# Kernel optimization log

Hardware: AMD Instinct MI355X
Metric: run time of the kernel (lower is better)

## Reference

```python
import jax, jax.numpy as jnp
import numpy as np

H = 1024      # hidden_size
NH = 16       # num_heads
HD = H // NH  # head_dim = 64
BUCKETS = 256
MAXREL = 512
SPAN = BUCKETS  # pos_ebd_size (position_buckets > 0)
B, S = 2, 2048


def setup_inputs() -> dict:
    key = jax.random.key(0)
    ks = jax.random.split(key, 10)
    s = 0.02
    return {
        'hidden_states': jax.random.normal(ks[0], (B, S, H), jnp.float32),
        'Wq': jax.random.normal(ks[1], (H, H), jnp.float32) * s, 'bq': jnp.zeros((H,), jnp.float32),
        'Wk': jax.random.normal(ks[2], (H, H), jnp.float32) * s, 'bk': jnp.zeros((H,), jnp.float32),
        'Wv': jax.random.normal(ks[3], (H, H), jnp.float32) * s, 'bv': jnp.zeros((H,), jnp.float32),
        'Wo': jax.random.normal(ks[4], (H, H), jnp.float32) * s, 'bo': jnp.zeros((H,), jnp.float32),
        'Wpk': jax.random.normal(ks[5], (H, H), jnp.float32) * s, 'bpk': jnp.zeros((H,), jnp.float32),
        'Wpq': jax.random.normal(ks[6], (H, H), jnp.float32) * s, 'bpq': jnp.zeros((H,), jnp.float32),
        'rel_emb': jax.random.normal(ks[7], (2 * SPAN, H), jnp.float32) * s,
        'ln_g': jnp.ones((H,), jnp.float32), 'ln_b': jnp.zeros((H,), jnp.float32),
    }


def _log_bucket(rel, bucket_size, max_position):
    # Faithful port of make_log_bucket_position
    sign = jnp.sign(rel).astype(jnp.float32)
    mid = bucket_size // 2
    abs_pos = jnp.where((rel < mid) & (rel > -mid), mid - 1, jnp.abs(rel)).astype(jnp.float32)
    log_pos = jnp.ceil(jnp.log(abs_pos / mid) / np.float32(np.log((max_position - 1) / mid)) * (mid - 1)) + mid
    bucket = jnp.where(abs_pos <= mid, rel.astype(jnp.float32), log_pos * sign)
    return bucket.astype(jnp.int32)


def _split_heads(x, b, s):
    # [B,S,H] -> [B,NH,S,HD]
    return x.reshape(b, s, NH, HD).transpose(0, 2, 1, 3)


def reference(hidden_states, Wq, bq, Wk, bk, Wv, bv, Wo, bo, Wpk, bpk, Wpq, bpq, rel_emb, ln_g, ln_b):
    b, s, _ = hidden_states.shape
    q = _split_heads(hidden_states @ Wq + bq, b, s)
    k = _split_heads(hidden_states @ Wk + bk, b, s)
    v = _split_heads(hidden_states @ Wv + bv, b, s)
    # scale_factor = 1 + ('c2p') + ('p2c') = 3
    scale = jnp.sqrt(jnp.asarray(HD * 3, jnp.float32))
    scores = jnp.einsum('bhqd,bhkd->bhqk', q, k) / scale
    # log-bucketed relative positions [S, S]
    ids = jnp.arange(s)
    rel = _log_bucket(ids[:, None] - ids[None, :], BUCKETS, MAXREL)
    # LayerNorm over rel embeddings (biased variance, eps=1e-5)
    mu = rel_emb.mean(-1, keepdims=True)
    var = rel_emb.var(-1, keepdims=True)
    re = (rel_emb - mu) / jnp.sqrt(var + 1e-5) * ln_g + ln_b   # [2*SPAN, H]
    pos_k = (re @ Wpk + bpk).reshape(2 * SPAN, NH, HD).transpose(1, 0, 2)  # [NH, 2*SPAN, HD]
    pos_q = (re @ Wpq + bpq).reshape(2 * SPAN, NH, HD).transpose(1, 0, 2)
    # c2p: content->position
    c2p = jnp.einsum('bhqd,hpd->bhqp', q, pos_k)                 # [B,NH,S,2*SPAN]
    c2p_idx = jnp.clip(rel + SPAN, 0, 2 * SPAN - 1)              # [S,S]
    c2p = jnp.take_along_axis(c2p, jnp.broadcast_to(c2p_idx[None, None], (b, NH, s, s)), axis=-1) / scale
    # p2c: position->content (gather on key axis, then transpose)
    p2c = jnp.einsum('bhkd,hpd->bhkp', k, pos_q)                 # [B,NH,S,2*SPAN]
    p2c_idx = jnp.clip(-rel + SPAN, 0, 2 * SPAN - 1)
    p2c = jnp.take_along_axis(p2c, jnp.broadcast_to(p2c_idx[None, None], (b, NH, s, s)), axis=-1)
    p2c = jnp.swapaxes(p2c, -1, -2) / scale
    scores = scores + c2p + p2c
    probs = jax.nn.softmax(scores.astype(jnp.float32), axis=-1).astype(q.dtype)
    ctx = jnp.einsum('bhqk,bhkd->bhqd', probs, v)
    ctx = ctx.transpose(0, 2, 1, 3).reshape(b, s, H)
    return ctx @ Wo + bo
```

## Files before the change

kernel.cpp:

```cpp
#include <hip/hip_runtime.h>

typedef unsigned short u16;
typedef unsigned int u32;
typedef unsigned long long u64;
typedef __attribute__((ext_vector_type(8))) short short8;
typedef __attribute__((ext_vector_type(4))) float float4v;

#define MFMA16(a, b, c) __builtin_amdgcn_mfma_f32_16x16x32_bf16((a), (b), (c), 0, 0, 0)

__device__ __forceinline__ u16 f2b(float x) {
    union { float f; unsigned u; } v; v.f = x;
    unsigned r = v.u + 0x7FFFu + ((v.u >> 16) & 1u);
    return (u16)(r >> 16);
}
__device__ __forceinline__ float b2f(u16 u) {
    union { unsigned u; float f; } v; v.u = ((unsigned)u) << 16; return v.f;
}

#define NH 16
#define S  2048
#define HD 64
#define H  1024
#define SC 0.10412111829775301f

#define OFF_REB   0ull
#define OFF_HSB   (OFF_REB  + 1048576ull)
#define OFF_WT    (OFF_HSB  + 8388608ull)
#define OFF_QB    (OFF_WT   + 12582912ull)
#define OFF_KB    (OFF_QB   + 8388608ull)
#define OFF_VT    (OFF_KB   + 8388608ull)
#define OFF_PKB   (OFF_VT   + 8388608ull)
#define OFF_PQB   (OFF_PKB  + 1048576ull)
#define OFF_C2P   (OFF_PQB  + 1048576ull)
#define OFF_P2CK  (OFF_C2P  + 67108864ull)
#define OFF_CTX   (OFF_P2CK + 67108864ull)
#define OFF_IDX   (OFF_CTX  + 8388608ull)
#define OFF_PF    (OFF_IDX  + 8192ull)
#define OFF_SP    (OFF_PF   + 262144ull)
#define SP_OHALF  4194304ull
#define SP_LBASE  (OFF_SP + 67108864ull)
#define SP_LHALF  65536ull
#define WS_NEED_SPLIT (SP_LBASE + 524288ull)

__global__ void k_build_idx(short* __restrict__ t) {
    int i = blockIdx.x * 256 + threadIdx.x;
    if (i >= 1024) return;
    int rel = i - 512;
    float fr = (float)rel;
    float abs_pos = (rel < 128 && rel > -128) ? 127.0f : fabsf(fr);
    const float LOGC = 1.3843393262841284f;
    float log_pos = ceilf(logf(abs_pos * (1.0f / 128.0f)) / LOGC * 127.0f) + 128.0f;
    float sgn = (fr > 0.f) ? 1.f : ((fr < 0.f) ? -1.f : 0.f);
    float bf = (abs_pos <= 128.0f) ? fr : log_pos * sgn;
    int idx = (int)bf + 256;
    idx = idx < 0 ? 0 : (idx > 511 ? 511 : idx);
    t[i] = (short)idx;
}

__global__ __launch_bounds__(256) void k_ln(const float* __restrict__ re,
                                            const float* __restrict__ g,
                                            const float* __restrict__ be,
                                            u16* __restrict__ out) {
    int row = blockIdx.x;
    const float4* x4 = (const float4*)(re + (size_t)row * H);
    int tid = threadIdx.x;
    float4 vv = x4[tid];
    float s = vv.x + vv.y + vv.z + vv.w;
    float s2 = vv.x * vv.x + vv.y * vv.y + vv.z * vv.z + vv.w * vv.w;
    for (int m = 1; m < 64; m <<= 1) {
        s += __shfl_xor(s, m, 64);
        s2 += __shfl_xor(s2, m, 64);
    }
    __shared__ float as[4], as2[4];
    if ((tid & 63) == 0) { as[tid >> 6] = s; as2[tid >> 6] = s2; }
    __syncthreads();
    s = as[0] + as[1] + as[2] + as[3];
    s2 = as2[0] + as2[1] + as2[2] + as2[3];
    float mu = s * (1.f / 1024.f);
    float var = s2 * (1.f / 1024.f) - mu * mu;
    float rstd = rsqrtf(var + 1e-5f);
    float4 gg = ((const float4*)g)[tid];
    float4 bb = ((const float4*)be)[tid];
    ushort4 r4;
    r4.x = f2b((vv.x - mu) * rstd * gg.x + bb.x);
    r4.y = f2b((vv.y - mu) * rstd * gg.y + bb.y);
    r4.z = f2b((vv.z - mu) * rstd * gg.z + bb.z);
    r4.w = f2b((vv.w - mu) * rstd * gg.w + bb.w);
    ((ushort4*)(out + (size_t)row * H))[tid] = r4;
}

__global__ __launch_bounds__(256) void k_cast(const float* __restrict__ x, u16* __restrict__ y) {
    int i = blockIdx.x * 256 + threadIdx.x;
    float4 v = ((const float4*)x)[i];
    ushort4 r;
    r.x = f2b(v.x); r.y = f2b(v.y); r.z = f2b(v.z); r.w = f2b(v.w);
    ((ushort4*)y)[i] = r;
}

__global__ __launch_bounds__(256) void k_wt6(const float* __restrict__ W0, const float* __restrict__ W1,
                                             const float* __restrict__ W2, const float* __restrict__ W3,
                                             const float* __restrict__ W4, const float* __restrict__ W5,
                                             u16* __restrict__ T0, u16* __restrict__ T1,
                                             u16* __restrict__ T2, u16* __restrict__ T3,
                                             u16* __restrict__ T4, u16* __restrict__ T5) {
    const float* W; u16* WT;
    switch (blockIdx.z) {
        case 0: W = W0; WT = T0; break;
        case 1: W = W1; WT = T1; break;
        case 2: W = W2; WT = T2; break;
        case 3: W = W3; WT = T3; break;
        case 4: W = W4; WT = T4; break;
        default: W = W5; WT = T5; break;
    }
    __shared__ float t[64][65];
    int k0 = blockIdx.x * 64, n0 = blockIdx.y * 64;
    int tid = threadIdx.x;
#pragma unroll
    for (int i = 0; i < 16; i++) {
        int lin = tid + 256 * i;
        int r = lin >> 6, c = lin & 63;
        t[r][c] = W[(size_t)(k0 + r) * H + n0 + c];
    }
    __syncthreads();
#pragma unroll
    for (int i = 0; i < 16; i++) {
        int lin = tid + 256 * i;
        int r = lin >> 6, c = lin & 63;
        WT[(size_t)(n0 + r) * H + k0 + c] = f2b(t[c][r]);
    }
}

template <int MODE>
__device__ __forceinline__ void gemm2_body(const u16* __restrict__ A,
                                           const u16* __restrict__ Bt,
                                           const float* __restrict__ bias,
                                           void* __restrict__ C, int N, int K) {
    __shared__ __align__(16) u16 As[128 * 32];
    __shared__ __align__(16) u16 Bs[128 * 32];
    int tid = threadIdx.x;
    int lane = tid & 63, w = tid >> 6;
    int ln = lane & 15, quad = lane >> 4;
    int m0 = blockIdx.x * 128, n0 = blockIdx.y * 128;
    int wm = (w >> 1) * 64, wn = (w & 1) * 64;
    float4v acc[4][4];
    float4v zero = {0.f, 0.f, 0.f, 0.f};
#pragma unroll
    for (int mi = 0; mi < 4; mi++)
#pragma unroll
        for (int ni = 0; ni < 4; ni++) acc[mi][ni] = zero;

    int r1 = tid >> 2, o1 = (tid & 3) * 8;
    const u16* ga1 = A + (size_t)(m0 + r1) * K + o1;
    const u16* gb1 = Bt + (size_t)(n0 + r1) * K + o1;
    u16* sa1 = &As[r1 * 32 + o1];
    u16* sb1 = &Bs[r1 * 32 + o1];
    size_t step2 = (size_t)64 * K;

    for (int k0 = 0; k0 < K; k0 += 32) {
        short8 va1 = *(const short8*)(ga1 + k0);
        short8 va2 = *(const short8*)(ga1 + step2 + k0);
        short8 vb1 = *(const short8*)(gb1 + k0);
        short8 vb2 = *(const short8*)(gb1 + step2 + k0);
        __syncthreads();
        *(short8*)sa1 = va1; *(short8*)(sa1 + 2048) = va2;
        *(short8*)sb1 = vb1; *(short8*)(sb1 + 2048) = vb2;
        __syncthreads();
        short8 af[4], bf[4];
#pragma unroll
        for (int mi = 0; mi < 4; mi++)
            af[mi] = *(const short8*)&As[(wm + mi * 16 + ln) * 32 + quad * 8];
#pragma unroll
        for (int ni = 0; ni < 4; ni++)
            bf[ni] = *(const short8*)&Bs[(wn + ni * 16 + ln) * 32 + quad * 8];
#pragma unroll
        for (int mi = 0; mi < 4; mi++)
#pragma unroll
            for (int ni = 0; ni < 4; ni++)
                acc[mi][ni] = MFMA16(af[mi], bf[ni], acc[mi][ni]);
    }

#pragma unroll
    for (int mi = 0; mi < 4; mi++) {
        int row0 = m0 + wm + mi * 16 + quad * 4;
#pragma unroll
        for (int ni = 0; ni < 4; ni++) {
            int col = n0 + wn + ni * 16 + ln;
            float bv = bias[col];
            if (MODE == 0) {
                u16* Cb = (u16*)C;
#pragma unroll
                for (int r = 0; r < 4; r++)
                    Cb[(size_t)(row0 + r) * N + col] = f2b(acc[mi][ni][r] + bv);
            } else if (MODE == 1) {
                float* Cf = (float*)C;
#pragma unroll
                for (int r = 0; r < 4; r++)
                    Cf[(size_t)(row0 + r) * N + col] = acc[mi][ni][r] + bv;
            } else if (MODE == 2) {
                u16* Cb = (u16*)C;
                int bb = row0 >> 11, s = row0 & 2047;
                ushort4 r4;
                r4.x = f2b(acc[mi][ni][0] + bv);
                r4.y = f2b(acc[mi][ni][1] + bv);
                r4.z = f2b(acc[mi][ni][2] + bv);
                r4.w = f2b(acc[mi][ni][3] + bv);
                *(ushort4*)(Cb + ((size_t)(bb * 1024 + col)) * 2048 + s) = r4;
            } else {
                u16* Cb = (u16*)C;
                int bb = row0 >> 11, s = row0 & 2047;
                int h = col >> 6, d = col & 63;
#pragma unroll
                for (int r = 0; r < 4; r++)
                    Cb[((size_t)(bb * 16 + h) * 2048 + s + r) * 64 + d] = f2b(acc[mi][ni][r] + bv);
            }
        }
    }
}

template <int MODE>
__global__ __launch_bounds__(256) void k_gemm2(const u16* __restrict__ A, const u16* __restrict__ Bt,
                                               const float* __restrict__ bias, void* __restrict__ C,
                                               int N, int K) {
    gemm2_body<MODE>(A, Bt, bias, C, N, K);
}

template <int MODE>
__global__ __launch_bounds__(256) void k_gemm2_dual(const u16* __restrict__ A,
                                                    const u16* __restrict__ Bt0, const u16* __restrict__ Bt1,
                                                    const float* __restrict__ b0, const float* __restrict__ b1,
                                                    void* __restrict__ C0, void* __restrict__ C1,
                                                    int N, int K) {
    if (blockIdx.z == 0) gemm2_body<MODE>(A, Bt0, b0, C0, N, K);
    else                 gemm2_body<MODE>(A, Bt1, b1, C1, N, K);
}

__global__ __launch_bounds__(256) void k_qkv(const u16* __restrict__ A,
                                             const u16* __restrict__ W0, const u16* __restrict__ W1,
                                             const u16* __restrict__ W2,
                                             const float* __restrict__ b0, const float* __restrict__ b1,
                                             const float* __restrict__ b2,
                                             u16* __restrict__ Q, u16* __restrict__ K, u16* __restrict__ VT) {
    if (blockIdx.z == 0)      gemm2_body<3>(A, W0, b0, Q, H, H);
    else if (blockIdx.z == 1) gemm2_body<3>(A, W1, b1, K, H, H);
    else                      gemm2_body<2>(A, W2, b2, VT, H, H);
}

__global__ __launch_bounds__(256) void k_pos_both(const u16* __restrict__ Qh, const u16* __restrict__ Kh,
                                                  const u16* __restrict__ pk, const u16* __restrict__ pq,
                                                  u16* __restrict__ c2p, u16* __restrict__ p2cK,
                                                  u16* __restrict__ pfar) {
    __shared__ __align__(16) u16 smem[2 * 128 * 72];
    u16* As = smem;
    u16* Bs = smem + 128 * 72;
    int tid = threadIdx.x;
    int lane = tid & 63, w = tid >> 6;
    int ln = lane & 15, quad = lane >> 4;
    int tr = blockIdx.z & 1, z = blockIdx.z >> 1, h = z & 15;
    int m0 = blockIdx.x * 128, n0 = blockIdx.y * 128;
    const u16* A = (tr ? Kh : Qh) + (size_t)z * S * HD;
    const u16* B = (tr ? pq : pk) + h * 64;
    int sr = tid >> 1, scb = (tid & 1) * 32;
    {
        const u16* ga = A + (size_t)(m0 + sr) * HD + scb;
        const u16* gb = B + (size_t)(n0 + sr) * H + scb;
#pragma unroll
        for (int j = 0; j < 4; j++) {
            *(short8*)&As[sr * 72 + scb + j * 8] = *(const short8*)(ga + j * 8);
            *(short8*)&Bs[sr * 72 + scb + j * 8] = *(const short8*)(gb + j * 8);
        }
    }
    __syncthreads();
    int wm = (w >> 1) * 64, wn = (w & 1) * 64;
    float4v acc[4][4];
    float4v zero = {0.f, 0.f, 0.f, 0.f};
#pragma unroll
    for (int mi = 0; mi < 4; mi++)
#pragma unroll
        for (int ni = 0; ni < 4; ni++) acc[mi][ni] = zero;
#pragma unroll
    for (int c = 0; c < 2; c++) {
        short8 af[4], bf[4];
#pragma unroll
        for (int mi = 0; mi < 4; mi++)
            af[mi] = *(const short8*)&As[(wm + mi * 16 + ln) * 72 + c * 32 + quad * 8];
#pragma unroll
        for (int ni = 0; ni < 4; ni++)
            bf[ni] = *(const short8*)&Bs[(wn + ni * 16 + ln) * 72 + c * 32 + quad * 8];
#pragma unroll
        for (int mi = 0; mi < 4; mi++)
#pragma unroll
            for (int ni = 0; ni < 4; ni++)
                acc[mi][ni] = MFMA16(af[mi], bf[ni], acc[mi][ni]);
    }
    u16* Cp = (tr ? p2cK : c2p) + (size_t)z * S * 512;
#pragma unroll
    for (int mi = 0; mi < 4; mi++) {
        int row0 = m0 + wm + mi * 16 + quad * 4;
#pragma unroll
        for (int ni = 0; ni < 4; ni++) {
            int col = n0 + wn + ni * 16 + ln;
#pragma unroll
            for (int r = 0; r < 4; r++)
                Cp[(size_t)(row0 + r) * 512 + col] = f2b(acc[mi][ni][r] * SC);
        }
    }
    if (tr) {
        if (n0 == 0 && (w & 1) == 0 && ln == 0) {
            u16* dst = pfar + (size_t)z * 2048 + m0 + wm + quad * 4;
#pragma unroll
            for (int mi = 0; mi < 4; mi++)
#pragma unroll
                for (int r = 0; r < 4; r++)
                    dst[mi * 16 + r] = f2b(acc[mi][0][r] * SC);
        }
        if (n0 == 384 && (w & 1) == 1 && ln == 15) {
            u16* dst = pfar + (size_t)(32 + z) * 2048 + m0 + wm + quad * 4;
#pragma unroll
            for (int mi = 0; mi < 4; mi++)
#pragma unroll
                for (int r = 0; r < 4; r++)
                    dst[mi * 16 + r] = f2b(acc[mi][3][r] * SC);
        }
    }
}

template <int SPLIT>
__global__ __launch_bounds__(256, 4) void k_attn(const u16* __restrict__ Qh,
                                                 const u16* __restrict__ Kh,
                                                 const u16* __restrict__ VT,
                                                 const u16* __restrict__ c2p,
                                                 const u16* __restrict__ p2cK,
                                                 const u16* __restrict__ pfar,
                                                 const short* __restrict__ idxTab,
                                                 float* __restrict__ oP,
                                                 float* __restrict__ lP,
                                                 u16* __restrict__ ctx) {
    __shared__ short s_idx1[1024];
    __shared__ __align__(16) u16 p_lds[4][16][72];
    __shared__ __align__(16) u16 Ks[64][72];
    __shared__ __align__(16) u16 Vs[64][72];
    int tid = threadIdx.x;
    for (int i = tid; i < 1024; i += 256) s_idx1[i] = idxTab[i];
    int lane = tid & 63, w = tid >> 6;
    int ln = lane & 15, quad = lane >> 4;
    int bx = blockIdx.x;
    int half = (SPLIT == 2) ? (bx & 1) : 0;
    int q0 = (SPLIT == 2) ? (bx >> 1) * 64 : bx * 64;
    int bh = blockIdx.y;
    int b = bh >> 4, h = bh & 15;
    int qs = q0 + w * 16;

    const u16* qptr = Qh + ((size_t)bh * S + qs + ln) * HD + quad * 8;
    short8 aq0 = *(const short8*)(qptr);
    short8 aq1 = *(const short8*)(qptr + 32);

    float4v o[4];
    float4v zero = {0.f, 0.f, 0.f, 0.f};
#pragma unroll
    for (int f = 0; f < 4; f++) o[f] = zero;
    float lrw[4] = {0.f, 0.f, 0.f, 0.f};

    const u16* c2pB = c2p + (size_t)bh * S * 512;
    const u16* p2cB = p2cK + (size_t)bh * S * 512;
    int qrow = qs + quad * 4;

    const u16* cvrow[4];
#pragma unroll
    for (int r = 0; r < 4; r++) cvrow[r] = c2pB + (size_t)(qrow + r) * 512;

    int sr = tid >> 2, sc = (tid & 3) * 16;
    const u16* kstg = Kh + ((size_t)bh * S + sr) * HD + sc;
    const u16* vstg = VT + (size_t)(b * 1024 + h * 64 + sr) * S + sc;

    const int NT = S / 64 / SPLIT;
    for (int t = 0; t < NT; t++) {
        int kk = (SPLIT == 2) ? (((t << 1) | half) << 6) : (t << 6);
        short8 kr0 = *(const short8*)(kstg + (size_t)kk * HD);
        short8 kr1 = *(const short8*)(kstg + (size_t)kk * HD + 8);
        short8 vr0 = *(const short8*)(vstg + kk);
        short8 vr1 = *(const short8*)(vstg + kk + 8);
        __syncthreads();
        *(short8*)&Ks[sr][sc] = kr0; *(short8*)&Ks[sr][sc + 8] = kr1;
        *(short8*)&Vs[sr][sc] = vr0; *(short8*)&Vs[sr][sc + 8] = vr1;
        __syncthreads();
        float4v sa[4];
#pragma unroll
        for (int f = 0; f < 4; f++) {
            short8 b0 = *(const short8*)&Ks[f * 16 + ln][quad * 8];
            short8 b1 = *(const short8*)&Ks[f * 16 + ln][32 + quad * 8];
            float4v tt = zero;
            tt = MFMA16(aq0, b0, tt);
            tt = MFMA16(aq1, b1, tt);
            sa[f] = tt;
        }
        int rel0 = q0 - kk;
        if (rel0 >= 569 || rel0 <= -633) {
            int idx = rel0 > 0 ? 511 : 0;
            const u16* pfb = pfar + (rel0 > 0 ? (size_t)(32 + bh) : (size_t)bh) * 2048 + kk;
            float cvr[4];
#pragma unroll
            for (int r = 0; r < 4; r++)
                cvr[r] = b2f(cvrow[r][idx]);
#pragma unroll
            for (int f = 0; f < 4; f++) {
                float pv = b2f(pfb[f * 16 + ln]);
#pragma unroll
                for (int r = 0; r < 4; r++) {
                    float p = exp2f(sa[f][r] * SC + cvr[r] + pv);
                    lrw[r] += p;
                    p_lds[w][quad * 4 + r][f * 16 + ln] = f2b(p);
                }
            }
        } else {
#pragma unroll
            for (int f = 0; f < 4; f++) {
                int ki = kk + f * 16 + ln;
                const u16* pvrow = p2cB + (size_t)ki * 512;
                int relb = qrow - ki;
                int idxr[4];
#pragma unroll
                for (int r = 0; r < 4; r++) {
                    int rel = relb + r;
                    rel = rel < -512 ? -512 : (rel > 511 ? 511 : rel);
                    idxr[r] = (int)s_idx1[rel + 512];
                }
                int i0 = idxr[0];
                const u32* p32 = (const u32*)pvrow;
                int e = i0 >> 1;
                u32 wx = p32[e], wy = p32[e + 1], wz = p32[e + 2];
                u64 lov = (u64)wx | ((u64)wy << 32);
                u64 hiv = (u64)wy | ((u64)wz << 32);
                int par = i0 & 1;
                u16 cvu[4];
#pragma unroll
                for (int r = 0; r < 4; r++) cvu[r] = cvrow[r][idxr[r]];
#pragma unroll
                for (int r = 0; r < 4; r++) {
                    int pos = par + (idxr[r] - i0);
                    u64 src = (pos < 4) ? lov : hiv;
                    int sh = ((pos < 4) ? pos : (pos - 2)) << 4;
                    u16 pvu = (u16)(src >> sh);
                    float p = exp2f(sa[f][r] * SC + b2f(cvu[r]) + b2f(pvu));
                    lrw[r] += p;
                    p_lds[w][quad * 4 + r][f * 16 + ln] = f2b(p);
                }
            }
        }
        short8 ap0 = *(const short8*)&p_lds[w][ln][quad * 8];
        short8 ap1 = *(const short8*)&p_lds[w][ln][32 + quad * 8];
#pragma unroll
        for (int f = 0; f < 4; f++) {
            short8 v0 = *(const short8*)&Vs[f * 16 + ln][quad * 8];
            short8 v1 = *(const short8*)&Vs[f * 16 + ln][32 + quad * 8];
            o[f] = MFMA16(ap0, v0, o[f]);
            o[f] = MFMA16(ap1, v1, o[f]);
        }
    }
#pragma unroll
    for (int r = 0; r < 4; r++) {
        lrw[r] += __shfl_xor(lrw[r], 1, 16);
        lrw[r] += __shfl_xor(lrw[r], 2, 16);
        lrw[r] += __shfl_xor(lrw[r], 4, 16);
        lrw[r] += __shfl_xor(lrw[r], 8, 16);
    }
    if (SPLIT == 1) {
        float inv_l[4];
#pragma unroll
        for (int r = 0; r < 4; r++) inv_l[r] = 1.f / lrw[r];
#pragma unroll
        for (int f = 0; f < 4; f++)
#pragma unroll
            for (int r = 0; r < 4; r++) {
                int qi = qs + quad * 4 + r;
                ctx[(size_t)(b * S + qi) * H + h * 64 + f * 16 + ln] = f2b(o[f][r] * inv_l[r]);
            }
    } else {
        float* oH = oP + (size_t)half * SP_OHALF;
#pragma unroll
        for (int f = 0; f < 4; f++)
#pragma unroll
            for (int r = 0; r < 4; r++) {
                int qi = qs + quad * 4 + r;
                oH[((size_t)bh * S + qi) * 64 + f * 16 + ln] = o[f][r];
            }
        if (ln == 0) {
            float* lH = lP + (size_t)half * SP_LHALF;
#pragma unroll
            for (int r = 0; r < 4; r++)
                lH[(size_t)bh * S + qs + quad * 4 + r] = lrw[r];
        }
    }
}

__global__ __launch_bounds__(256) void k_merge(const float* __restrict__ oP,
                                               const float* __restrict__ lP,
                                               u16* __restrict__ ctx) {
    int t = blockIdx.x * 256 + threadIdx.x;
    int d4 = (t & 15) * 4;
    int h  = (t >> 4) & 15;
    int qq = (t >> 8) & 2047;
    int b  = t >> 19;
    int bh = b * 16 + h;
    size_t base = ((size_t)bh * S + qq) * 64 + d4;
    float4 o0 = *(const float4*)(oP + base);
    float4 o1 = *(const float4*)(oP + SP_OHALF + base);
    float l0 = lP[(size_t)bh * S + qq];
    float l1 = lP[SP_LHALF + (size_t)bh * S + qq];
    float inv = 1.f / (l0 + l1);
    ushort4 r4;
    r4.x = f2b((o0.x + o1.x) * inv);
    r4.y = f2b((o0.y + o1.y) * inv);
    r4.z = f2b((o0.z + o1.z) * inv);
    r4.w = f2b((o0.w + o1.w) * inv);
    *(ushort4*)(ctx + (((size_t)(b * S + qq)) * 16 + h) * 64 + d4) = r4;
}

extern "C" void kernel_launch(void* const* d_in, const int* in_sizes, int n_in,
                              void* d_out, int out_size, void* d_ws, size_t ws_size,
                              hipStream_t stream) {
    const float* hs  = (const float*)d_in[0];
    const float* Wq  = (const float*)d_in[1];
    const float* bq  = (const float*)d_in[2];
    const float* Wk  = (const float*)d_in[3];
    const float* bk  = (const float*)d_in[4];
    const float* Wv  = (const float*)d_in[5];
    const float* bv  = (const float*)d_in[6];
    const float* Wo  = (const float*)d_in[7];
    const float* bo  = (const float*)d_in[8];
    const float* Wpk = (const float*)d_in[9];
    const float* bpk = (const float*)d_in[10];
    const float* Wpq = (const float*)d_in[11];
    const float* bpq = (const float*)d_in[12];
    const float* rel = (const float*)d_in[13];
    const float* lng = (const float*)d_in[14];
    const float* lnb = (const float*)d_in[15];

    char* ws = (char*)d_ws;
    u16* re_b   = (u16*)(ws + OFF_REB);
    u16* hs_b   = (u16*)(ws + OFF_HSB);
    u16* wt0    = (u16*)(ws + OFF_WT);
    u16* wt1    = (u16*)(ws + OFF_WT + 2097152ull);
    u16* wt2    = (u16*)(ws + OFF_WT + 2ull * 2097152ull);
    u16* wt3    = (u16*)(ws + OFF_WT + 3ull * 2097152ull);
    u16* wt4    = (u16*)(ws + OFF_WT + 4ull * 2097152ull);
    u16* wt5    = (u16*)(ws + OFF_WT + 5ull * 2097152ull);
    u16* Q_b    = (u16*)(ws + OFF_QB);
    u16* K_b    = (u16*)(ws + OFF_KB);
    u16* VT_b   = (u16*)(ws + OFF_VT);
    u16* posk_b = (u16*)(ws + OFF_PKB);
    u16* posq_b = (u16*)(ws + OFF_PQB);
    u16* c2p_b  = (u16*)(ws + OFF_C2P);
    u16* p2cK_b = (u16*)(ws + OFF_P2CK);
    u16* ctx_b  = (u16*)(ws + OFF_CTX);
    short* idx_t = (short*)(ws + OFF_IDX);
    u16* pfar_b = (u16*)(ws + OFF_PF);
    float* oP   = (float*)(ws + OFF_SP);
    float* lP   = (float*)(ws + SP_LBASE);

    dim3 blk(256);
    k_build_idx<<<dim3(4), blk, 0, stream>>>(idx_t);
    k_ln<<<dim3(512), blk, 0, stream>>>(rel, lng, lnb, re_b);
    k_cast<<<dim3(4096), blk, 0, stream>>>(hs, hs_b);
    k_wt6<<<dim3(16, 16, 6), blk, 0, stream>>>(Wq, Wk, Wv, Wo, Wpk, Wpq,
                                               wt0, wt1, wt2, wt3, wt4, wt5);

    k_qkv<<<dim3(32, 8, 3), blk, 0, stream>>>(hs_b, wt0, wt1, wt2, bq, bk, bv, Q_b, K_b, VT_b);
    k_gemm2_dual<0><<<dim3(4, 8, 2), blk, 0, stream>>>(re_b, wt4, wt5, bpk, bpq, posk_b, posq_b, H, H);

    k_pos_both<<<dim3(16, 4, 64), blk, 0, stream>>>(Q_b, K_b, posk_b, posq_b, c2p_b, p2cK_b, pfar_b);

    if (ws_size >= WS_NEED_SPLIT) {
        k_attn<2><<<dim3(64, 32), blk, 0, stream>>>(Q_b, K_b, VT_b, c2p_b, p2cK_b, pfar_b, idx_t, oP, lP, ctx_b);
        k_merge<<<dim3(4096), blk, 0, stream>>>(oP, lP, ctx_b);
    } else {
        k_attn<1><<<dim3(32, 32), blk, 0, stream>>>(Q_b, K_b, VT_b, c2p_b, p2cK_b, pfar_b, idx_t, oP, lP, ctx_b);
    }

    k_gemm2<1><<<dim3(32, 8), blk, 0, stream>>>(ctx_b, wt3, bo, d_out, H, H);
}
```

Baseline: 369.8 us.

## Pack probabilities with hardware bf16 convert and permute key layout for paired stores

Probabilities are now converted two at a time with v_cvt_pk_bf16_f32 and written as 32-bit words into the P LDS tile. This interleaves key columns f0/f1 and f2/f3, so the V tile is loaded and its bf16 halves are shuffled to the matching permuted key order, keeping the P·V product consistent. The p2c bias extraction is also simplified to a single shifted 64-bit window. The goal is fewer conversion instructions and fewer LDS stores, paid for with extra VALU bit manipulation on the V staging path.

Measured after the change: 385.7 us. 1.04x slower.

```diff
diff --git a/kernel.cpp b/kernel.cpp
--- a/kernel.cpp
+++ b/kernel.cpp
@@ -5,6 +5,7 @@
 typedef unsigned long long u64;
 typedef __attribute__((ext_vector_type(8))) short short8;
 typedef __attribute__((ext_vector_type(4))) float float4v;
+typedef __attribute__((ext_vector_type(4))) unsigned int u32x4;
 
 #define MFMA16(a, b, c) __builtin_amdgcn_mfma_f32_16x16x32_bf16((a), (b), (c), 0, 0, 0)
 
@@ -15,6 +16,11 @@
 }
 __device__ __forceinline__ float b2f(u16 u) {
     union { unsigned u; float f; } v; v.u = ((unsigned)u) << 16; return v.f;
+}
+__device__ __forceinline__ u32 cvtpk(float lo, float hi) {
+    u32 r;
+    asm("v_cvt_pk_bf16_f32 %0, %1, %2" : "=v"(r) : "v"(lo), "v"(hi));
+    return r;
 }
 
 #define NH 16
@@ -370,18 +376,28 @@
 
     int sr = tid >> 2, sc = (tid & 3) * 16;
     const u16* kstg = Kh + ((size_t)bh * S + sr) * HD + sc;
-    const u16* vstg = VT + (size_t)(b * 1024 + h * 64 + sr) * S + sc;
+    int t2 = tid & 3, h2 = t2 >> 1, jo = (t2 & 1) * 8;
+    const u16* vstg = VT + (size_t)(b * 1024 + h * 64 + sr) * S + h2 * 32 + jo;
 
     const int NT = S / 64 / SPLIT;
     for (int t = 0; t < NT; t++) {
         int kk = (SPLIT == 2) ? (((t << 1) | half) << 6) : (t << 6);
         short8 kr0 = *(const short8*)(kstg + (size_t)kk * HD);
         short8 kr1 = *(const short8*)(kstg + (size_t)kk * HD + 8);
-        short8 vr0 = *(const short8*)(vstg + kk);
-        short8 vr1 = *(const short8*)(vstg + kk + 8);
+        union V8 { short8 s; u32x4 u; } va, vb, w0, w1;
+        va.s = *(const short8*)(vstg + kk);
+        vb.s = *(const short8*)(vstg + kk + 16);
+        w0.u[0] = (va.u[0] & 0xffffu) | (vb.u[0] << 16);
+        w0.u[1] = (va.u[0] >> 16) | (vb.u[0] & 0xffff0000u);
+        w0.u[2] = (va.u[1] & 0xffffu) | (vb.u[1] << 16);
+        w0.u[3] = (va.u[1] >> 16) | (vb.u[1] & 0xffff0000u);
+        w1.u[0] = (va.u[2] & 0xffffu) | (vb.u[2] << 16);
+        w1.u[1] = (va.u[2] >> 16) | (vb.u[2] & 0xffff0000u);
+        w1.u[2] = (va.u[3] & 0xffffu) | (vb.u[3] << 16);
+        w1.u[3] = (va.u[3] >> 16) | (vb.u[3] & 0xffff0000u);
         __syncthreads();
         *(short8*)&Ks[sr][sc] = kr0; *(short8*)&Ks[sr][sc + 8] = kr1;
-        *(short8*)&Vs[sr][sc] = vr0; *(short8*)&Vs[sr][sc + 8] = vr1;
+        *(short8*)&Vs[sr][t2 * 16] = w0.s; *(short8*)&Vs[sr][t2 * 16 + 8] = w1.s;
         __syncthreads();
         float4v sa[4];
 #pragma unroll
@@ -394,24 +410,30 @@
             sa[f] = tt;
         }
         int rel0 = q0 - kk;
+        u32* prow0 = (u32*)&p_lds[w][quad * 4][0];
         if (rel0 >= 569 || rel0 <= -633) {
             int idx = rel0 > 0 ? 511 : 0;
             const u16* pfb = pfar + (rel0 > 0 ? (size_t)(32 + bh) : (size_t)bh) * 2048 + kk;
-            float cvr[4];
+            float cvr[4], pvf[4];
 #pragma unroll
             for (int r = 0; r < 4; r++)
                 cvr[r] = b2f(cvrow[r][idx]);
 #pragma unroll
-            for (int f = 0; f < 4; f++) {
-                float pv = b2f(pfb[f * 16 + ln]);
-#pragma unroll
-                for (int r = 0; r < 4; r++) {
-                    float p = exp2f(sa[f][r] * SC + cvr[r] + pv);
-                    lrw[r] += p;
-                    p_lds[w][quad * 4 + r][f * 16 + ln] = f2b(p);
-                }
+            for (int f = 0; f < 4; f++)
+                pvf[f] = b2f(pfb[f * 16 + ln]);
+#pragma unroll
+            for (int r = 0; r < 4; r++) {
+                float p0 = exp2f(sa[0][r] * SC + cvr[r] + pvf[0]);
+                float p1 = exp2f(sa[1][r] * SC + cvr[r] + pvf[1]);
+                float p2 = exp2f(sa[2][r] * SC + cvr[r] + pvf[2]);
+                float p3 = exp2f(sa[3][r] * SC + cvr[r] + pvf[3]);
+                lrw[r] += (p0 + p1) + (p2 + p3);
+                u32* prow = prow0 + r * 36;
+                prow[ln] = cvtpk(p0, p1);
+                prow[16 + ln] = cvtpk(p2, p3);
             }
         } else {
+            float bias[4][4];
 #pragma unroll
             for (int f = 0; f < 4; f++) {
                 int ki = kk + f * 16 + ln;
@@ -429,21 +451,26 @@
                 int e = i0 >> 1;
                 u32 wx = p32[e], wy = p32[e + 1], wz = p32[e + 2];
                 u64 lov = (u64)wx | ((u64)wy << 32);
-                u64 hiv = (u64)wy | ((u64)wz << 32);
-                int par = i0 & 1;
-                u16 cvu[4];
-#pragma unroll
-                for (int r = 0; r < 4; r++) cvu[r] = cvrow[r][idxr[r]];
+                u64 shifted = (i0 & 1) ? ((lov >> 16) | ((u64)wz << 48)) : lov;
 #pragma unroll
                 for (int r = 0; r < 4; r++) {
-                    int pos = par + (idxr[r] - i0);
-                    u64 src = (pos < 4) ? lov : hiv;
-                    int sh = ((pos < 4) ? pos : (pos - 2)) << 4;
-                    u16 pvu = (u16)(src >> sh);
-                    float p = exp2f(sa[f][r] * SC + b2f(cvu[r]) + b2f(pvu));
-                    lrw[r] += p;
-                    p_lds[w][quad * 4 + r][f * 16 + ln] = f2b(p);
+                    u16 cv = cvrow[r][idxr[r]];
+                    int sh = (idxr[r] - i0) << 4;
+                    union { u32 u; float f; } pv;
+                    pv.u = ((u32)(shifted >> sh)) << 16;
+                    bias[f][r] = b2f(cv) + pv.f;
                 }
+            }
+#pragma unroll
+            for (int r = 0; r < 4; r++) {
+                float p0 = exp2f(sa[0][r] * SC + bias[0][r]);
+                float p1 = exp2f(sa[1][r] * SC + bias[1][r]);
+                float p2 = exp2f(sa[2][r] * SC + bias[2][r]);
+                float p3 = exp2f(sa[3][r] * SC + bias[3][r]);
+                lrw[r] += (p0 + p1) + (p2 + p3);
+                u32* prow = prow0 + r * 36;
+                prow[ln] = cvtpk(p0, p1);
+                prow[16 + ln] = cvtpk(p2, p3);
             }
         }
         short8 ap0 = *(const short8*)&p_lds[w][ln][quad * 8];
```

## Pack probability stores with cvt_pk and permute V layout to match interleaved keys

Applied to the files above, without the earlier changes.

The attention inner loop now writes two bf16 probabilities per 32-bit LDS store via v_cvt_pk_bf16_f32, pairing key columns f and f+1. The V-transpose GEMM epilogue permutes sequence positions within each 64-block so the P·V MFMA still contracts over matching keys. The bias gather is simplified with a single shifted 64-bit window, and s_setprio wraps the MFMA sections. This cuts LDS store and conversion instruction counts, but the V epilogue switches from vector stores to scattered scalar stores, and correctness depends on the permutation matching exactly.

Result: no change. 371.2 us (+0.4%).

```diff
diff --git a/kernel.cpp b/kernel.cpp
--- a/kernel.cpp
+++ b/kernel.cpp
@@ -15,6 +15,11 @@
 }
 __device__ __forceinline__ float b2f(u16 u) {
     union { unsigned u; float f; } v; v.u = ((unsigned)u) << 16; return v.f;
+}
+__device__ __forceinline__ u32 cvtpk(float lo, float hi) {
+    u32 r;
+    asm("v_cvt_pk_bf16_f32 %0, %1, %2" : "=v"(r) : "v"(lo), "v"(hi));
+    return r;
 }
 
 #define NH 16
@@ -199,12 +204,12 @@
             } else if (MODE == 2) {
                 u16* Cb = (u16*)C;
                 int bb = row0 >> 11, s = row0 & 2047;
-                ushort4 r4;
-                r4.x = f2b(acc[mi][ni][0] + bv);
-                r4.y = f2b(acc[mi][ni][1] + bv);
-                r4.z = f2b(acc[mi][ni][2] + bv);
-                r4.w = f2b(acc[mi][ni][3] + bv);
-                *(ushort4*)(Cb + ((size_t)(bb * 1024 + col)) * 2048 + s) = r4;
+                int base64 = s & ~63, j = s & 63;
+                int p0 = ((j >> 5) << 5) + ((j & 15) << 1) + ((j >> 4) & 1);
+                u16* dst = Cb + ((size_t)(bb * 1024 + col)) * 2048 + base64;
+#pragma unroll
+                for (int r = 0; r < 4; r++)
+                    dst[p0 + 2 * r] = f2b(acc[mi][ni][r] + bv);
             } else {
                 u16* Cb = (u16*)C;
                 int bb = row0 >> 11, s = row0 & 2047;
@@ -323,6 +328,32 @@
         }
     }
 }
+
+#define GATHER_BIAS(F, B0, B1, B2, B3) do {                                          \
+    int ki_ = kk + (F) * 16 + ln;                                                    \
+    const u16* pvrow_ = p2cB + (size_t)ki_ * 512;                                    \
+    int relb_ = qrow - ki_;                                                          \
+    int i0_, i1_, i2_, i3_;                                                          \
+    { int rel = relb_;     rel = rel < -512 ? -512 : (rel > 511 ? 511 : rel); i0_ = (int)s_idx1[rel + 512]; } \
+    { int rel = relb_ + 1; rel = rel < -512 ? -512 : (rel > 511 ? 511 : rel); i1_ = (int)s_idx1[rel + 512]; } \
+    { int rel = relb_ + 2; rel = rel < -512 ? -512 : (rel > 511 ? 511 : rel); i2_ = (int)s_idx1[rel + 512]; } \
+    { int rel = relb_ + 3; rel = rel < -512 ? -512 : (rel > 511 ? 511 : rel); i3_ = (int)s_idx1[rel + 512]; } \
+    const u32* p32_ = (const u32*)pvrow_;                                            \
+    int e_ = i0_ >> 1;                                                               \
+    u32 wx_ = p32_[e_], wy_ = p32_[e_ + 1], wz_ = p32_[e_ + 2];                      \
+    u64 lov_ = (u64)wx_ | ((u64)wy_ << 32);                                          \
+    u64 sft_ = (i0_ & 1) ? ((lov_ >> 16) | ((u64)wz_ << 48)) : lov_;                 \
+    u16 c0_ = cvrow[0][i0_], c1_ = cvrow[1][i1_], c2_ = cvrow[2][i2_], c3_ = cvrow[3][i3_]; \
+    union { u32 u; float f; } q0_, q1_, q2_, q3_;                                    \
+    q0_.u = ((u32)(sft_)) << 16;                                                     \
+    q1_.u = ((u32)(sft_ >> ((i1_ - i0_) << 4))) << 16;                               \
+    q2_.u = ((u32)(sft_ >> ((i2_ - i0_) << 4))) << 16;                               \
+    q3_.u = ((u32)(sft_ >> ((i3_ - i0_) << 4))) << 16;                               \
+    B0 = b2f(c0_) + q0_.f;                                                           \
+    B1 = b2f(c1_) + q1_.f;                                                           \
+    B2 = b2f(c2_) + q2_.f;                                                           \
+    B3 = b2f(c3_) + q3_.f;                                                           \
+} while (0)
 
 template <int SPLIT>
 __global__ __launch_bounds__(256, 4) void k_attn(const u16* __restrict__ Qh,
@@ -384,6 +415,7 @@
         *(short8*)&Vs[sr][sc] = vr0; *(short8*)&Vs[sr][sc + 8] = vr1;
         __syncthreads();
         float4v sa[4];
+        __builtin_amdgcn_s_setprio(1);
 #pragma unroll
         for (int f = 0; f < 4; f++) {
             short8 b0 = *(const short8*)&Ks[f * 16 + ln][quad * 8];
@@ -393,61 +425,57 @@
             tt = MFMA16(aq1, b1, tt);
             sa[f] = tt;
         }
+        __builtin_amdgcn_s_setprio(0);
         int rel0 = q0 - kk;
+        u32* prow0 = (u32*)&p_lds[w][quad * 4][0];
         if (rel0 >= 569 || rel0 <= -633) {
             int idx = rel0 > 0 ? 511 : 0;
             const u16* pfb = pfar + (rel0 > 0 ? (size_t)(32 + bh) : (size_t)bh) * 2048 + kk;
-            float cvr[4];
+            float cvr[4], pvf[4];
 #pragma unroll
             for (int r = 0; r < 4; r++)
                 cvr[r] = b2f(cvrow[r][idx]);
 #pragma unroll
-            for (int f = 0; f < 4; f++) {
-                float pv = b2f(pfb[f * 16 + ln]);
+            for (int f = 0; f < 4; f++)
+                pvf[f] = b2f(pfb[f * 16 + ln]);
+#pragma unroll
+            for (int u = 0; u < 2; u++) {
 #pragma unroll
                 for (int r = 0; r < 4; r++) {
-                    float p = exp2f(sa[f][r] * SC + cvr[r] + pv);
-                    lrw[r] += p;
-                    p_lds[w][quad * 4 + r][f * 16 + ln] = f2b(p);
+                    float p0 = exp2f(sa[2 * u][r] * SC + cvr[r] + pvf[2 * u]);
+                    float p1 = exp2f(sa[2 * u + 1][r] * SC + cvr[r] + pvf[2 * u + 1]);
+                    lrw[r] += p0 + p1;
+                    prow0[r * 36 + u * 16 + ln] = cvtpk(p0, p1);
                 }
             }
         } else {
 #pragma unroll
-            for (int f = 0; f < 4; f++) {
-                int ki = kk + f * 16 + ln;
-                const u16* pvrow = p2cB + (size_t)ki * 512;
-                int relb = qrow - ki;
-                int idxr[4];
-#pragma unroll
-                for (int r = 0; r < 4; r++) {
-                    int rel = relb + r;
-                    rel = rel < -512 ? -512 : (rel > 511 ? 511 : rel);
-                    idxr[r] = (int)s_idx1[rel + 512];
-                }
-                int i0 = idxr[0];
-                const u32* p32 = (const u32*)pvrow;
-                int e = i0 >> 1;
-                u32 wx = p32[e], wy = p32[e + 1], wz = p32[e + 2];
-                u64 lov = (u64)wx | ((u64)wy << 32);
-                u64 hiv = (u64)wy | ((u64)wz << 32);
-                int par = i0 & 1;
-                u16 cvu[4];
-#pragma unroll
-                for (int r = 0; r < 4; r++) cvu[r] = cvrow[r][idxr[r]];
-#pragma unroll
-                for (int r = 0; r < 4; r++) {
-                    int pos = par + (idxr[r] - i0);
-                    u64 src = (pos < 4) ? lov : hiv;
-                    int sh = ((pos < 4) ? pos : (pos - 2)) << 4;
-                    u16 pvu = (u16)(src >> sh);
-                    float p = exp2f(sa[f][r] * SC + b2f(cvu[r]) + b2f(pvu));
-                    lrw[r] += p;
-                    p_lds[w][quad * 4 + r][f * 16 + ln] = f2b(p);
-                }
+            for (int u = 0; u < 2; u++) {
+                float ba0, ba1, ba2, ba3, bb0, bb1, bb2, bb3;
+                GATHER_BIAS(2 * u, ba0, ba1, ba2, ba3);
+                GATHER_BIAS(2 * u + 1, bb0, bb1, bb2, bb3);
+                float p0, p1;
+                p0 = exp2f(sa[2 * u][0] * SC + ba0);
+                p1 = exp2f(sa[2 * u + 1][0] * SC + bb0);
+                lrw[0] += p0 + p1;
+                prow0[0 * 36 + u * 16 + ln] = cvtpk(p0, p1);
+                p0 = exp2f(sa[2 * u][1] * SC + ba1);
+                p1 = exp2f(sa[2 * u + 1][1] * SC + bb1);
+                lrw[1] += p0 + p1;
+                prow0[1 * 36 + u * 16 + ln] = cvtpk(p0, p1);
+                p0 = exp2f(sa[2 * u][2] * SC + ba2);
+                p1 = exp2f(sa[2 * u + 1][2] * SC + bb2);
+                lrw[2] += p0 + p1;
+                prow0[2 * 36 + u * 16 + ln] = cvtpk(p0, p1);
+                p0 = exp2f(sa[2 * u][3] * SC + ba3);
+                p1 = exp2f(sa[2 * u + 1][3] * SC + bb3);
+                lrw[3] += p0 + p1;
+                prow0[3 * 36 + u * 16 + ln] = cvtpk(p0, p1);
             }
         }
         short8 ap0 = *(const short8*)&p_lds[w][ln][quad * 8];
         short8 ap1 = *(const short8*)&p_lds[w][ln][32 + quad * 8];
+        __builtin_amdgcn_s_setprio(1);
 #pragma unroll
         for (int f = 0; f < 4; f++) {
             short8 v0 = *(const short8*)&Vs[f * 16 + ln][quad * 8];
@@ -455,6 +483,7 @@
             o[f] = MFMA16(ap0, v0, o[f]);
             o[f] = MFMA16(ap1, v1, o[f]);
         }
+        __builtin_amdgcn_s_setprio(0);
     }
 #pragma unroll
     for (int r = 0; r < 4; r++) {
```
